# Kernel tuning notes

Hardware: AMD Instinct MI355X
Metric: run time of the kernel (lower is better)

## Reference

```python
import jax, jax.numpy as jnp
import numpy as np

EMB = 768
HEADS = 12
HEAD_DIM = EMB // HEADS  # 64
SCALE = 1.0 / float(np.sqrt(EMB))  # NOTE: source divides by sqrt(emb_size), not sqrt(head_dim)


def setup_inputs() -> dict:
    key = jax.random.key(0)
    k_x, k_wqkv, k_bqkv, k_wp, k_bp = jax.random.split(key, 5)
    b, n = 4, 2048
    x = jax.random.normal(k_x, (b, n, EMB), dtype=jnp.float32)
    # torch Linear default init ~ U(-1/sqrt(in), 1/sqrt(in)); scale doesn't matter for correctness baseline
    lim = 1.0 / np.sqrt(EMB)
    W_qkv = jax.random.uniform(k_wqkv, (EMB, 3 * EMB), minval=-lim, maxval=lim, dtype=jnp.float32)
    b_qkv = jax.random.uniform(k_bqkv, (3 * EMB,), minval=-lim, maxval=lim, dtype=jnp.float32)
    W_proj = jax.random.uniform(k_wp, (EMB, EMB), minval=-lim, maxval=lim, dtype=jnp.float32)
    b_proj = jax.random.uniform(k_bp, (EMB,), minval=-lim, maxval=lim, dtype=jnp.float32)
    return {"x": x, "W_qkv": W_qkv, "b_qkv": b_qkv, "W_proj": W_proj, "b_proj": b_proj}


def reference(x, W_qkv, b_qkv, W_proj, b_proj):
    b, n, _ = x.shape
    qkv = x @ W_qkv + b_qkv                              # [b, n, 3*emb]
    # rearrange 'b n (h d qkv) -> qkv b h n d' : qkv is the innermost split
    qkv = qkv.reshape(b, n, HEADS, HEAD_DIM, 3)
    qkv = jnp.transpose(qkv, (4, 0, 2, 1, 3))            # [3, b, h, n, d]
    q, k, v = qkv[0], qkv[1], qkv[2]
    att = jnp.einsum('bhnd,bhmd->bhnm', q, k) * SCALE    # [b, h, n, n]
    att = jax.nn.softmax(att, axis=-1)
    # dropout is identity at inference
    out = jnp.einsum('bhnm,bhmd->bhnd', att, v)          # [b, h, n, d]
    out = jnp.transpose(out, (0, 2, 1, 3)).reshape(b, n, EMB)  # 'b h n d -> b n (h d)'
    return out @ W_proj + b_proj
```

## Files before the change

kernel.cpp:

```cpp
#include <hip/hip_runtime.h>
#include <math.h>

typedef _Float16 f16x8 __attribute__((ext_vector_type(8)));
typedef _Float16 f16x4 __attribute__((ext_vector_type(4)));
typedef _Float16 f16x2 __attribute__((ext_vector_type(2)));
typedef float f32x4 __attribute__((ext_vector_type(4)));
typedef float f32x16 __attribute__((ext_vector_type(16)));
typedef unsigned int uint32;
typedef unsigned int uint32x4 __attribute__((ext_vector_type(4)));
typedef unsigned short ushort16;

static constexpr int EMB_ = 768;
static constexpr int NH_ = 12;
static constexpr int HD_ = 64;
static constexpr int SEQ_ = 2048;
static constexpr int B_ = 4;
static constexpr float QSCALE_ = 0.036084391824351615f * 1.4426950408889634f;

__device__ __forceinline__ void gload_lds16(const void* g, void* l) {
    __builtin_amdgcn_global_load_lds((const __attribute__((address_space(1))) void*)g,
                                     (__attribute__((address_space(3))) void*)l,
                                     16, 0, 0);
}

__global__ __launch_bounds__(256)
void prep_k(const float* __restrict__ W0, _Float16* __restrict__ Wt0,
            const float* __restrict__ W1, _Float16* __restrict__ Wt1,
            const float* __restrict__ x, _Float16* __restrict__ xh,
            const float* __restrict__ bq, float* __restrict__ bqP,
            int C0, int C1, int n4)
{
    const int tid = threadIdx.x;
    if (blockIdx.z == 2) {
        if (blockIdx.y == 0 && blockIdx.x < 9) {
            const int c = blockIdx.x * 256 + tid;
            const int h = c / 192, rem = c - h * 192;
            const int d = rem / 3, s = rem - d * 3;
            bqP[s * 768 + h * 64 + d] = bq[c];
        }
        const int stride = 72 * 24 * 256;
        for (int i = (blockIdx.y * 72 + blockIdx.x) * 256 + tid; i < n4; i += stride) {
            float4 v = ((const float4*)x)[i];
            f16x4 o = {(_Float16)v.x, (_Float16)v.y, (_Float16)v.z, (_Float16)v.w};
            ((f16x4*)xh)[i] = o;
        }
        return;
    }
    const float* W; _Float16* Wt; int C;
    if (blockIdx.z == 0) { W = W0; Wt = Wt0; C = C0; }
    else                 { W = W1; Wt = Wt1; C = C1; }
    const int c0 = blockIdx.x * 32;
    if (c0 >= C) return;
    const int r0 = blockIdx.y * 32;
    __shared__ float ls[32][33];
    const int tc = tid & 31, tr = tid >> 5;
    const bool perm = (blockIdx.z == 0);
#pragma unroll
    for (int i = 0; i < 4; ++i)
        ls[tr + 8 * i][tc] = W[(size_t)(r0 + tr + 8 * i) * C + c0 + tc];
    __syncthreads();
#pragma unroll
    for (int i = 0; i < 4; ++i) {
        const int c = c0 + tr + 8 * i;
        int cp = c;
        if (perm) {
            const int h = c / 192, rem = c - h * 192;
            const int d = rem / 3, s = rem - d * 3;
            cp = s * 768 + h * 64 + d;
        }
        Wt[(size_t)cp * EMB_ + r0 + tc] = (_Float16)ls[tc][tr + 8 * i];
    }
}

template<int EPI>
__global__ __launch_bounds__(256, 2)
void gemm16(const _Float16* __restrict__ A, const _Float16* __restrict__ Bt,
            const float* __restrict__ bias, float* __restrict__ outF,
            _Float16* __restrict__ hq, _Float16* __restrict__ hk,
            _Float16* __restrict__ hv,
            int M, int N, int K)
{
    __shared__ __align__(16) _Float16 As[128 * 64];
    __shared__ __align__(16) _Float16 Bs[128 * 64];

    const int tid  = threadIdx.x;
    const int lane = tid & 63;
    const int w    = tid >> 6;
    const int txm  = lane & 15, g = lane >> 4;
    const int wr   = w >> 1, wc = w & 1;
    const int m0   = blockIdx.y * 128, n0 = blockIdx.x * 128;
    const int nk   = K >> 6;

    const int sr  = lane >> 3;
    const int scX = (((lane & 7) ^ sr) << 3);
    const _Float16* gA[4]; const _Float16* gB[4];
    _Float16* lA[4]; _Float16* lB[4];
#pragma unroll
    for (int i = 0; i < 4; ++i) {
        const int row = w * 32 + 8 * i;
        gA[i] = A  + (size_t)(m0 + row + sr) * K + scX;
        gB[i] = Bt + (size_t)(n0 + row + sr) * K + scX;
        lA[i] = As + row * 64 + lane * 8;
        lB[i] = Bs + row * 64 + lane * 8;
    }

    f32x4 acc[4][4];
#pragma unroll
    for (int i = 0; i < 4; ++i)
#pragma unroll
        for (int j = 0; j < 4; ++j) acc[i][j] = (f32x4){0.f, 0.f, 0.f, 0.f};

    const int fsw = txm & 7;

    for (int kt = 0; kt < nk; ++kt) {
        __syncthreads();
#pragma unroll
        for (int i = 0; i < 4; ++i) gload_lds16(gA[i] + kt * 64, lA[i]);
#pragma unroll
        for (int i = 0; i < 4; ++i) gload_lds16(gB[i] + kt * 64, lB[i]);
        __syncthreads();

#pragma unroll
        for (int kh = 0; kh < 2; ++kh) {
            const int coff = ((4 * kh + g) ^ fsw) << 3;
            f16x8 af[4], bf[4];
#pragma unroll
            for (int i = 0; i < 4; ++i)
                af[i] = *(const f16x8*)&As[(wr * 64 + 16 * i + txm) * 64 + coff];
#pragma unroll
            for (int j = 0; j < 4; ++j)
                bf[j] = *(const f16x8*)&Bs[(wc * 64 + 16 * j + txm) * 64 + coff];
#pragma unroll
            for (int i = 0; i < 4; ++i)
#pragma unroll
                for (int j = 0; j < 4; ++j)
                    acc[i][j] = __builtin_amdgcn_mfma_f32_16x16x32_f16(af[i], bf[j], acc[i][j], 0, 0, 0);
        }
    }

    if (EPI == 0) {
        const int s  = (n0 >= 1536) ? 2 : (n0 >= 768 ? 1 : 0);
        _Float16* bse = (s == 0) ? hq : (s == 1) ? hk : hv;
        const float scl = (s == 0) ? QSCALE_ : 1.f;
        const int nb = n0 - s * 768;
#pragma unroll
        for (int i = 0; i < 4; ++i) {
            const int mB = m0 + wr * 64 + 16 * i + 4 * g;
#pragma unroll
            for (int j = 0; j < 4; ++j) {
                const int nc = wc * 64 + 16 * j + txm;
                const float bv = bias[n0 + nc];
                const int np = nb + nc;
                const int h  = np >> 6;
                const int dd = np & 63;
#pragma unroll
                for (int r = 0; r < 4; ++r) {
                    const int mm = mB + r;
                    const int bb = mm >> 11;
                    const int nn = mm & (SEQ_ - 1);
                    const int ddE = (s == 1) ? (dd ^ ((nn & 7) * 8)) : dd;
                    bse[(((size_t)(bb * NH_ + h)) * SEQ_ + nn) * HD_ + ddE] =
                        (_Float16)((acc[i][j][r] + bv) * scl);
                }
            }
        }
    } else {
#pragma unroll
        for (int i = 0; i < 4; ++i) {
#pragma unroll
            for (int r = 0; r < 4; ++r) {
                const int mm = m0 + wr * 64 + 16 * i + 4 * g + r;
                float* dst = outF + (size_t)mm * N + n0 + wc * 64 + txm;
#pragma unroll
                for (int j = 0; j < 4; ++j)
                    dst[16 * j] = acc[i][j][r] + bias[n0 + wc * 64 + 16 * j + txm];
            }
        }
    }
}

__global__ __launch_bounds__(256, 3)
void attn_k(const _Float16* __restrict__ Qb, const _Float16* __restrict__ Kb,
            const _Float16* __restrict__ Vb, _Float16* __restrict__ Out)
{
    __shared__ __align__(16) _Float16 Ks[2][64][64];
    __shared__ __align__(16) _Float16 Vs[2][64][72];

    const int tid  = threadIdx.x;
    const int lane = tid & 63;
    const int wv   = tid >> 6;
    const int l31  = lane & 31;
    const int h    = lane >> 5;

    const int lin  = blockIdx.x;
    const int slot = lin >> 3;
    const int bh   = (lin & 7) + 8 * (slot >> 4);
    const int q0   = (slot & 15) << 7;
    const int bb   = bh / NH_;
    const int hh   = bh - bb * NH_;

    const _Float16* KpB = Kb + (size_t)bh * SEQ_ * HD_;
    const _Float16* VpB = Vb + (size_t)bh * SEQ_ * HD_;

    auto kstage = [&](int buf, int kt) {
        const int c0 = kt << 6;
#pragma unroll
        for (int i = 0; i < 2; ++i)
            gload_lds16(KpB + (size_t)(c0 + 16 * wv + 8 * i) * HD_ + lane * 8,
                        &Ks[buf][16 * wv + 8 * i][0] + lane * 8);
    };
    kstage(0, 0);

    f16x8 qf[4];
    {
        const _Float16* Qrow = Qb + ((size_t)bh * SEQ_ + q0 + 32 * wv + l31) * HD_;
#pragma unroll
        for (int ks = 0; ks < 4; ++ks)
            qf[ks] = *(const f16x8*)(Qrow + 16 * ks + 8 * h);
    }

    const int vc = (tid & 31) << 1;
    const int vd = (tid >> 5) << 3;
    const int swz7 = l31 & 7;

    f32x16 o2[2];
#pragma unroll
    for (int dt2 = 0; dt2 < 2; ++dt2)
#pragma unroll
        for (int r = 0; r < 16; ++r) o2[dt2][r] = 0.f;
    float li = 0.f;

    uint4 va = *(const uint4*)(VpB + (size_t)vc * HD_ + vd);
    uint4 vb = *(const uint4*)(VpB + (size_t)(vc + 1) * HD_ + vd);

    constexpr int NT = SEQ_ / 64;
    for (int kt = 0; kt < NT; ++kt) {
        const int buf = kt & 1;
        {
            const ushort16* pa = (const ushort16*)&va;
            const ushort16* pb = (const ushort16*)&vb;
#pragma unroll
            for (int j = 0; j < 8; ++j) {
                uint32 wrd = (uint32)pa[j] | ((uint32)pb[j] << 16);
                *(uint32*)&Vs[buf][vd + j][vc] = wrd;
            }
        }
        __syncthreads();

        if (kt + 1 < NT) {
            kstage(buf ^ 1, kt + 1);
            const int c0n = (kt + 1) << 6;
            va = *(const uint4*)(VpB + (size_t)(c0n + vc) * HD_ + vd);
            vb = *(const uint4*)(VpB + (size_t)(c0n + vc + 1) * HD_ + vd);
        }

        f32x16 st2[2];
#pragma unroll
        for (int ct2 = 0; ct2 < 2; ++ct2) {
#pragma unroll
            for (int r = 0; r < 16; ++r) st2[ct2][r] = 0.f;
            f16x8 kf[4];
            const int crow = 32 * ct2 + l31;
#pragma unroll
            for (int ks = 0; ks < 4; ++ks)
                kf[ks] = *(const f16x8*)&Ks[buf][crow][((2 * ks + h) ^ swz7) << 3];
#pragma unroll
            for (int ks = 0; ks < 4; ++ks)
                st2[ct2] = __builtin_amdgcn_mfma_f32_32x32x16_f16(kf[ks], qf[ks], st2[ct2], 0, 0, 0);
        }

        f16x8 pfrag[4];
#pragma unroll
        for (int ct2 = 0; ct2 < 2; ++ct2) {
            uint32 w[8];
#pragma unroll
            for (int m = 0; m < 8; ++m) {
                float p0 = __builtin_amdgcn_exp2f(st2[ct2][2 * m]);
                float p1 = __builtin_amdgcn_exp2f(st2[ct2][2 * m + 1]);
                li += p0 + p1;
                f16x2 t = {(_Float16)p0, (_Float16)p1};
                w[m] = __builtin_bit_cast(uint32, t);
            }
            asm("v_permlane32_swap_b32 %0, %1" : "+v"(w[0]), "+v"(w[2]));
            asm("v_permlane32_swap_b32 %0, %1" : "+v"(w[1]), "+v"(w[3]));
            asm("v_permlane32_swap_b32 %0, %1" : "+v"(w[4]), "+v"(w[6]));
            asm("v_permlane32_swap_b32 %0, %1" : "+v"(w[5]), "+v"(w[7]));
            uint32x4 lo = {w[0], w[1], w[2], w[3]};
            uint32x4 hi = {w[4], w[5], w[6], w[7]};
            pfrag[2 * ct2]     = __builtin_bit_cast(f16x8, lo);
            pfrag[2 * ct2 + 1] = __builtin_bit_cast(f16x8, hi);
        }

#pragma unroll
        for (int dt2 = 0; dt2 < 2; ++dt2) {
            f16x8 vf[4];
            const int drow = 32 * dt2 + l31;
#pragma unroll
            for (int kc = 0; kc < 4; ++kc)
                vf[kc] = *(const f16x8*)&Vs[buf][drow][16 * kc + 8 * h];
#pragma unroll
            for (int kc = 0; kc < 4; ++kc)
                o2[dt2] = __builtin_amdgcn_mfma_f32_32x32x16_f16(vf[kc], pfrag[kc], o2[dt2], 0, 0, 0);
        }
    }

    float rs = li + __shfl_xor(li, 32);
    const float inv = 1.f / rs;
    const int q = q0 + 32 * wv + l31;
    _Float16* dst = Out + ((size_t)bb * SEQ_ + q) * EMB_ + hh * HD_;
#pragma unroll
    for (int dt2 = 0; dt2 < 2; ++dt2)
#pragma unroll
        for (int r4 = 0; r4 < 4; ++r4) {
            f16x4 pk = {(_Float16)(o2[dt2][4 * r4 + 0] * inv), (_Float16)(o2[dt2][4 * r4 + 1] * inv),
                        (_Float16)(o2[dt2][4 * r4 + 2] * inv), (_Float16)(o2[dt2][4 * r4 + 3] * inv)};
            *(f16x4*)(dst + 32 * dt2 + 8 * r4 + 4 * h) = pk;
        }
}

extern "C" void kernel_launch(void* const* d_in, const int* in_sizes, int n_in,
                              void* d_out, int out_size, void* d_ws, size_t ws_size,
                              hipStream_t stream)
{
    const float* x    = (const float*)d_in[0];
    const float* Wqkv = (const float*)d_in[1];
    const float* bqkv = (const float*)d_in[2];
    const float* Wp   = (const float*)d_in[3];
    const float* bp   = (const float*)d_in[4];
    float* out = (float*)d_out;

    const size_t PER = (size_t)B_ * NH_ * SEQ_ * HD_;
    _Float16* Qh     = (_Float16*)d_ws;
    _Float16* Kh     = Qh + PER;
    _Float16* Vh     = Kh + PER;
    _Float16* xh     = Vh + PER;
    _Float16* WqkvT  = xh + (size_t)B_ * SEQ_ * EMB_;
    _Float16* WprojT = WqkvT + (size_t)EMB_ * 3 * EMB_;
    _Float16* Ah     = WprojT + (size_t)EMB_ * EMB_;
    float*    bqP    = (float*)(Ah + (size_t)B_ * SEQ_ * EMB_);

    const int M = B_ * SEQ_;

    prep_k<<<dim3(72, 24, 3), dim3(256), 0, stream>>>(
        Wqkv, WqkvT, Wp, WprojT, x, xh, bqkv, bqP, 3 * EMB_, EMB_, B_ * SEQ_ * EMB_ / 4);

    gemm16<0><<<dim3(3 * EMB_ / 128, M / 128), dim3(256), 0, stream>>>(
        xh, WqkvT, bqP, nullptr, Qh, Kh, Vh, M, 3 * EMB_, EMB_);

    attn_k<<<dim3((SEQ_ / 128) * B_ * NH_), dim3(256), 0, stream>>>(Qh, Kh, Vh, Ah);

    gemm16<1><<<dim3(EMB_ / 128, M / 128), dim3(256), 0, stream>>>(
        Ah, WprojT, bp, out, nullptr, nullptr, nullptr, M, EMB_, EMB_);
}
```

Before: 210.1 us.

## Stage V via async global-to-LDS loads and read with transposing ds_read_tr

```diff
diff --git a/kernel.cpp b/kernel.cpp
--- a/kernel.cpp
+++ b/kernel.cpp
@@ -8,7 +8,6 @@
 typedef float f32x16 __attribute__((ext_vector_type(16)));
 typedef unsigned int uint32;
 typedef unsigned int uint32x4 __attribute__((ext_vector_type(4)));
-typedef unsigned short ushort16;
 
 static constexpr int EMB_ = 768;
 static constexpr int NH_ = 12;
@@ -21,6 +20,13 @@
     __builtin_amdgcn_global_load_lds((const __attribute__((address_space(1))) void*)g,
                                      (__attribute__((address_space(3))) void*)l,
                                      16, 0, 0);
+}
+
+template<int OFF>
+__device__ __forceinline__ f16x4 tr16(uint32 a) {
+    f16x4 d;
+    asm volatile("ds_read_b64_tr_b16 %0, %1 offset:%2" : "=v"(d) : "v"(a), "i"(OFF));
+    return d;
 }
 
 __global__ __launch_bounds__(256)
@@ -184,13 +190,14 @@
             const _Float16* __restrict__ Vb, _Float16* __restrict__ Out)
 {
     __shared__ __align__(16) _Float16 Ks[2][64][64];
-    __shared__ __align__(16) _Float16 Vs[2][64][72];
+    __shared__ __align__(16) _Float16 Vs[2][4096];
 
     const int tid  = threadIdx.x;
     const int lane = tid & 63;
     const int wv   = tid >> 6;
     const int l31  = lane & 31;
     const int h    = lane >> 5;
+    const int txm  = lane & 15;
 
     const int lin  = blockIdx.x;
     const int slot = lin >> 3;
@@ -209,7 +216,17 @@
             gload_lds16(KpB + (size_t)(c0 + 16 * wv + 8 * i) * HD_ + lane * 8,
                         &Ks[buf][16 * wv + 8 * i][0] + lane * 8);
     };
+    const int laneG = (((lane >> 5) << 2) + ((lane >> 1) & 3)) * 64
+                    + ((lane >> 3) & 3) * 16 + (lane & 1) * 8;
+    auto vstage = [&](int buf, int kt) {
+        const int c064 = (kt << 6) * HD_;
+#pragma unroll
+        for (int i = 0; i < 2; ++i)
+            gload_lds16(VpB + c064 + wv * 1024 + i * 512 + laneG,
+                        &Vs[buf][wv * 1024 + i * 512]);
+    };
     kstage(0, 0);
+    vstage(0, 0);
 
     f16x8 qf[4];
     {
@@ -219,9 +236,14 @@
             qf[ks] = *(const f16x8*)(Qrow + 16 * ks + 8 * h);
     }
 
-    const int vc = (tid & 31) << 1;
-    const int vd = (tid >> 5) << 3;
     const int swz7 = l31 & 7;
+
+    uint32 vbase;
+    {
+        auto* p3 = (__attribute__((address_space(3))) _Float16*)&Vs[0][0];
+        vbase = (uint32)(uintptr_t)p3
+              + (uint32)(h * 1024 + ((l31 >> 4) & 1) * 128 + txm * 8);
+    }
 
     f32x16 o2[2];
 #pragma unroll
@@ -229,29 +251,15 @@
 #pragma unroll
         for (int r = 0; r < 16; ++r) o2[dt2][r] = 0.f;
     float li = 0.f;
-
-    uint4 va = *(const uint4*)(VpB + (size_t)vc * HD_ + vd);
-    uint4 vb = *(const uint4*)(VpB + (size_t)(vc + 1) * HD_ + vd);
 
     constexpr int NT = SEQ_ / 64;
     for (int kt = 0; kt < NT; ++kt) {
         const int buf = kt & 1;
-        {
-            const ushort16* pa = (const ushort16*)&va;
-            const ushort16* pb = (const ushort16*)&vb;
-#pragma unroll
-            for (int j = 0; j < 8; ++j) {
-                uint32 wrd = (uint32)pa[j] | ((uint32)pb[j] << 16);
-                *(uint32*)&Vs[buf][vd + j][vc] = wrd;
-            }
-        }
         __syncthreads();
 
         if (kt + 1 < NT) {
             kstage(buf ^ 1, kt + 1);
-            const int c0n = (kt + 1) << 6;
-            va = *(const uint4*)(VpB + (size_t)(c0n + vc) * HD_ + vd);
-            vb = *(const uint4*)(VpB + (size_t)(c0n + vc + 1) * HD_ + vd);
+            vstage(buf ^ 1, kt + 1);
         }
 
         f32x16 st2[2];
@@ -268,6 +276,15 @@
             for (int ks = 0; ks < 4; ++ks)
                 st2[ct2] = __builtin_amdgcn_mfma_f32_32x32x16_f16(kf[ks], qf[ks], st2[ct2], 0, 0, 0);
         }
+
+        f16x4 vt[2][4][2];
+        const uint32 vab = vbase + ((uint32)buf << 13);
+#define TRRD(d2, kc, jh) vt[d2][kc][jh] = tr16<((4*(kc)+(jh))*512 + (d2)*256)>(vab)
+        TRRD(0,0,0); TRRD(0,0,1); TRRD(0,1,0); TRRD(0,1,1);
+        TRRD(0,2,0); TRRD(0,2,1); TRRD(0,3,0); TRRD(0,3,1);
+        TRRD(1,0,0); TRRD(1,0,1); TRRD(1,1,0); TRRD(1,1,1);
+        TRRD(1,2,0); TRRD(1,2,1); TRRD(1,3,0); TRRD(1,3,1);
+#undef TRRD
 
         f16x8 pfrag[4];
 #pragma unroll
@@ -291,16 +308,17 @@
             pfrag[2 * ct2 + 1] = __builtin_bit_cast(f16x8, hi);
         }
 
+        asm volatile("s_waitcnt lgkmcnt(0)" ::: "memory");
+        __builtin_amdgcn_sched_barrier(0);
+
 #pragma unroll
         for (int dt2 = 0; dt2 < 2; ++dt2) {
-            f16x8 vf[4];
-            const int drow = 32 * dt2 + l31;
-#pragma unroll
-            for (int kc = 0; kc < 4; ++kc)
-                vf[kc] = *(const f16x8*)&Vs[buf][drow][16 * kc + 8 * h];
-#pragma unroll
-            for (int kc = 0; kc < 4; ++kc)
-                o2[dt2] = __builtin_amdgcn_mfma_f32_32x32x16_f16(vf[kc], pfrag[kc], o2[dt2], 0, 0, 0);
+#pragma unroll
+            for (int kc = 0; kc < 4; ++kc) {
+                f16x8 v8 = __builtin_shufflevector(vt[dt2][kc][0], vt[dt2][kc][1],
+                                                   0, 1, 2, 3, 4, 5, 6, 7);
+                o2[dt2] = __builtin_amdgcn_mfma_f32_32x32x16_f16(v8, pfrag[kc], o2[dt2], 0, 0, 0);
+            }
         }
     }
 
```

New measurement: 213.8 us (median of 2 runs). No clear change (+1.8%).
